# Performance work log

Measured on AMD Instinct MI355X. Metric: run time of the kernel, lower is better.

Reference implementation:

```python
import jax, jax.numpy as jnp
import numpy as np

B, L, H, HKV, D, E = 2, 2048, 8, 1, 256, 2048
SCALING = D ** -0.5


def rotate_half(x):
    x1, x2 = jnp.split(x, 2, axis=-1)
    return jnp.concatenate([-x2, x1], axis=-1)


def setup_inputs() -> dict:
    key = jax.random.key(0)
    ks = jax.random.split(key, 5)
    hidden_states = jax.random.normal(ks[0], (B, L, E), jnp.float32)
    attention_mask = jnp.zeros((B, 1, 1, L, L), jnp.float32)  # additive mask (all visible)
    # standard RoPE tables, shape [L, D]
    inv_freq = 1.0 / (10000.0 ** (jnp.arange(0, D, 2, dtype=jnp.float32) / D))
    freqs = jnp.arange(L, dtype=jnp.float32)[:, None] * inv_freq[None, :]
    emb = jnp.concatenate([freqs, freqs], axis=-1)
    cos, sin = jnp.cos(emb), jnp.sin(emb)
    s = 0.02
    Wq = jax.random.normal(ks[1], (H * D, E), jnp.float32) * s
    Wk = jax.random.normal(ks[2], (HKV * D, E), jnp.float32) * s
    Wv = jax.random.normal(ks[3], (HKV * D, E), jnp.float32) * s
    Wo = jax.random.normal(ks[4], (E, H * D), jnp.float32) * s
    return {"hidden_states": hidden_states, "attention_mask": attention_mask,
            "cos": cos, "sin": sin, "Wq": Wq, "Wk": Wk, "Wv": Wv, "Wo": Wo}


def reference(hidden_states, attention_mask, cos, sin, Wq, Wk, Wv, Wo):
    b, l, _ = hidden_states.shape
    q = jnp.einsum('ble,de->bld', hidden_states, Wq)
    k = jnp.einsum('ble,de->bld', hidden_states, Wk)
    v = jnp.einsum('ble,de->bld', hidden_states, Wv)
    # q: [B, L, 1, H, D] -> transpose(1,3) -> [B, H, 1, L, D]
    q = jnp.transpose(q.reshape(b, l, 1, H, D), (0, 3, 2, 1, 4))
    # k, v: [B, 1, L, Hkv, D] -> transpose(2,3) -> [B, 1, Hkv, L, D]
    k = jnp.transpose(k.reshape(b, 1, l, HKV, D), (0, 1, 3, 2, 4))
    v = jnp.transpose(v.reshape(b, 1, l, HKV, D), (0, 1, 3, 2, 4))
    # RoPE (cos/sin broadcast over leading dims)
    q = q * cos + rotate_half(q) * sin
    k = k * cos + rotate_half(k) * sin
    # scores: [B, H, Hkv, L, L]
    attn = jnp.matmul(q, jnp.swapaxes(k, -1, -2)) * SCALING
    attn = attn + attention_mask
    attn = jax.nn.softmax(attn.astype(jnp.float32), axis=-1)
    out = jnp.matmul(attn, v)                         # [B, H, Hkv, L, D]
    out = jnp.transpose(out, (0, 1, 3, 2, 4))         # [B, H, L, Hkv, D]
    out = out.reshape(b, l, H * D)                    # row-major reshape, as torch .reshape
    return jnp.einsum('bld,ed->ble', out, Wo)
```

## Files before the change

kernel.cpp:

```cpp
#include <hip/hip_runtime.h>

typedef unsigned short u16;
typedef __attribute__((ext_vector_type(8))) short short8;
typedef __attribute__((ext_vector_type(4))) float f32x4;

struct __align__(8) US4 { u16 x, y, z, w; };

__device__ __forceinline__ u16 f2bf(float x) {
  union { float f; unsigned u; } c; c.f = x;
  unsigned r = c.u + 0x7fffu + ((c.u >> 16) & 1u);
  return (u16)(r >> 16);
}
__device__ __forceinline__ float bf2f(u16 u) {
  union { unsigned u; float f; } c; c.u = ((unsigned)u) << 16;
  return c.f;
}
__device__ __forceinline__ void gload_lds16(const void* g, void* l) {
  __builtin_amdgcn_global_load_lds(
      (const __attribute__((address_space(1))) void*)g,
      (__attribute__((address_space(3))) void*)l, 16, 0, 0);
}
__device__ __forceinline__ f32x4 fzero4() {
  f32x4 z; z[0] = 0.f; z[1] = 0.f; z[2] = 0.f; z[3] = 0.f; return z;
}

__global__ __launch_bounds__(256) void cvt_all(
    const float* __restrict__ h, const float* __restrict__ wq,
    const float* __restrict__ wk, const float* __restrict__ wv,
    const float* __restrict__ wo, u16* __restrict__ Xbf,
    u16* __restrict__ Wqkv, u16* __restrict__ Wob) {
  int b = blockIdx.x;
  const float* s; u16* d; int off;
  if (b < 8192)       { s = h;  d = Xbf;            off = b; }
  else if (b < 12288) { s = wq; d = Wqkv;           off = b - 8192; }
  else if (b < 12800) { s = wk; d = Wqkv + 4194304; off = b - 12288; }
  else if (b < 13312) { s = wv; d = Wqkv + 4718592; off = b - 12800; }
  else                { s = wo; d = Wob;            off = b - 13312; }
  int i = (off * 256 + threadIdx.x) * 4;
  float4 v = *(const float4*)(s + i);
  US4 o = { f2bf(v.x), f2bf(v.y), f2bf(v.z), f2bf(v.w) };
  *(US4*)(d + i) = o;
}

template <int MODE>
__global__ __launch_bounds__(256) void gemm_nt(
    const u16* __restrict__ A, const u16* __restrict__ Bw,
    u16* __restrict__ q_out, u16* __restrict__ k_out, u16* __restrict__ v_out,
    float* __restrict__ c_out) {
  __shared__ u16 lA[128 * 32];
  __shared__ u16 lB[128 * 32];
  const int K = 2048;
  int t = threadIdx.x, w = t >> 6, lane = t & 63;
  int wm = w >> 1, wn = w & 1;
  int m0 = blockIdx.x * 128, n0 = blockIdx.y * 128;
  int g = lane >> 4, qi = lane & 15;

  f32x4 acc[4][4];
#pragma unroll
  for (int i = 0; i < 4; i++)
#pragma unroll
    for (int j = 0; j < 4; j++) acc[i][j] = fzero4();

  for (int k0 = 0; k0 < K; k0 += 32) {
#pragma unroll
    for (int i = 0; i < 2; i++) {
      int off = i * 4096 + w * 1024 + lane * 16;
      int row = off >> 6, cg = (off >> 4) & 3;
      gload_lds16(A + (size_t)(m0 + row) * K + k0 + cg * 8,
                  (char*)lA + i * 4096 + w * 1024);
      gload_lds16(Bw + (size_t)(n0 + row) * K + k0 + cg * 8,
                  (char*)lB + i * 4096 + w * 1024);
    }
    __syncthreads();
    short8 af[4], bfr[4];
#pragma unroll
    for (int f = 0; f < 4; f++) {
      int ra = wm * 64 + f * 16 + qi;
      int rb = wn * 64 + f * 16 + qi;
      int kb2 = g * 16;
      af[f] = *(const short8*)((const char*)lA + ra * 64 + kb2);
      bfr[f] = *(const short8*)((const char*)lB + rb * 64 + kb2);
    }
#pragma unroll
    for (int i = 0; i < 4; i++)
#pragma unroll
      for (int j = 0; j < 4; j++)
        acc[i][j] = __builtin_amdgcn_mfma_f32_16x16x32_bf16(af[i], bfr[j], acc[i][j], 0, 0, 0);
    __syncthreads();
  }

#pragma unroll
  for (int i = 0; i < 4; i++) {
#pragma unroll
    for (int j = 0; j < 4; j++) {
#pragma unroll
      for (int r = 0; r < 4; r++) {
        int m = m0 + wm * 64 + i * 16 + g * 4 + r;
        int n = n0 + wn * 64 + j * 16 + qi;
        float v = acc[i][j][r];
        if (MODE == 0) {
          int b = m >> 11, l = m & 2047;
          if (n < 2048) {
            int h = n >> 8, dd = n & 255;
            q_out[(((size_t)(b * 8 + h) * 2048) + l) * 256 + dd] = f2bf(v);
          } else if (n < 2304) {
            int dd = n - 2048;
            k_out[((size_t)b * 2048 + l) * 256 + dd] = f2bf(v);
          } else {
            int dd = n - 2304;
            v_out[((size_t)b * 256 + dd) * 2048 + l] = f2bf(v);
          }
        } else {
          c_out[(size_t)m * 2048 + n] = v;
        }
      }
    }
  }
}

__global__ __launch_bounds__(256) void rope_kernel(u16* __restrict__ q, u16* __restrict__ k,
                                                   const float* __restrict__ cosT,
                                                   const float* __restrict__ sinT) {
  int idx = blockIdx.x * 2 + (threadIdx.x >> 7);
  int d = threadIdx.x & 127;
  u16* ptr;
  int l;
  float sc;
  if (idx < 32768) { ptr = q + (size_t)idx * 256; l = idx & 2047; sc = 0.0625f; }
  else             { ptr = k + (size_t)(idx - 32768) * 256; l = (idx - 32768) & 2047; sc = 1.0f; }
  float x1 = bf2f(ptr[d]), x2 = bf2f(ptr[d + 128]);
  float c1 = cosT[l * 256 + d], s1 = sinT[l * 256 + d];
  float c2 = cosT[l * 256 + d + 128], s2 = sinT[l * 256 + d + 128];
  float o1 = (x1 * c1 - x2 * s1) * sc;
  float o2 = (x2 * c2 + x1 * s2) * sc;
  ptr[d] = f2bf(o1);
  ptr[d + 128] = f2bf(o2);
}

__global__ __launch_bounds__(256, 1) void flash_kernel(
    const u16* __restrict__ qr, const u16* __restrict__ kr,
    const u16* __restrict__ vt_g, u16* __restrict__ attnout) {
  __shared__ u16 kt[2][64 * 256];
  __shared__ u16 vt[2][256 * 64];
  __shared__ u16 pl[4][2048];

  int t = threadIdx.x, w = t >> 6, lane = t & 63;
  int qi = lane & 15, g = lane >> 4;
  int b = blockIdx.z, h = blockIdx.y;
  int bh = b * 8 + h;
  int l0 = blockIdx.x * 128 + w * 32;

  const u16* kb = kr + (size_t)b * (2048 * 256);
  const u16* vb = vt_g + (size_t)b * (256 * 2048);

  short8 qf[2][8];
#pragma unroll
  for (int qg = 0; qg < 2; qg++) {
    const u16* qbase = qr + ((size_t)bh * 2048 + l0 + qg * 16 + qi) * 256 + g * 8;
#pragma unroll
    for (int ks = 0; ks < 8; ks++) qf[qg][ks] = *(const short8*)(qbase + ks * 32);
  }

  f32x4 ot[16][2];
#pragma unroll
  for (int fd = 0; fd < 16; fd++) { ot[fd][0] = fzero4(); ot[fd][1] = fzero4(); }
  float mrow[2] = { -1e30f, -1e30f }, lrow[2] = { 0.f, 0.f };

  auto stage = [&](int buf, int kv) {
#pragma unroll
    for (int i = 0; i < 8; i++) {
      int off = i * 4096 + w * 1024 + lane * 16;
      int row = off >> 9, gc = (off >> 4) & 31;
      int gs = gc ^ (row & 7);
      gload_lds16(kb + (size_t)(kv + row) * 256 + gs * 8,
                  (char*)kt[buf] + i * 4096 + w * 1024);
    }
#pragma unroll
    for (int i = 0; i < 8; i++) {
      int off = i * 4096 + w * 1024 + lane * 16;
      int d = off >> 7, gc = (off >> 4) & 7;
      int gs = gc ^ (d & 7);
      gload_lds16(vb + (size_t)d * 2048 + kv + gs * 8,
                  (char*)vt[buf] + i * 4096 + w * 1024);
    }
  };

  stage(0, 0);
  __syncthreads();

  for (int tt = 0; tt < 32; ++tt) {
    int cur = tt & 1;
    if (tt < 31) stage(cur ^ 1, (tt + 1) * 64);

    f32x4 st[4][2];
    const char* kbase = (const char*)kt[cur];
#pragma unroll
    for (int f = 0; f < 4; f++) {
      st[f][0] = fzero4(); st[f][1] = fzero4();
      int row = f * 16 + qi;
#pragma unroll
      for (int ks = 0; ks < 8; ks++) {
        int slot = (4 * ks + g) ^ (row & 7);
        short8 kf = *(const short8*)(kbase + row * 512 + slot * 16);
        st[f][0] = __builtin_amdgcn_mfma_f32_16x16x32_bf16(kf, qf[0][ks], st[f][0], 0, 0, 0);
        st[f][1] = __builtin_amdgcn_mfma_f32_16x16x32_bf16(kf, qf[1][ks], st[f][1], 0, 0, 0);
      }
    }

#pragma unroll
    for (int qg = 0; qg < 2; qg++) {
      float tmax = -1e30f;
#pragma unroll
      for (int f = 0; f < 4; f++)
#pragma unroll
        for (int r = 0; r < 4; r++) tmax = fmaxf(tmax, st[f][qg][r]);
      tmax = fmaxf(tmax, __shfl_xor(tmax, 16));
      tmax = fmaxf(tmax, __shfl_xor(tmax, 32));
      float mnew = fmaxf(mrow[qg], tmax);
      float scale = __expf(mrow[qg] - mnew);
      float tsum = 0.f;
#pragma unroll
      for (int f = 0; f < 4; f++)
#pragma unroll
        for (int r = 0; r < 4; r++) {
          float p = __expf(st[f][qg][r] - mnew);
          st[f][qg][r] = p;
          tsum += p;
        }
      tsum += __shfl_xor(tsum, 16);
      tsum += __shfl_xor(tsum, 32);
      lrow[qg] = lrow[qg] * scale + tsum;
      mrow[qg] = mnew;
#pragma unroll
      for (int fd = 0; fd < 16; fd++)
#pragma unroll
        for (int r = 0; r < 4; r++) ot[fd][qg][r] *= scale;

      int qrow = qg * 16 + qi;
#pragma unroll
      for (int f = 0; f < 4; f++) {
        US4 pw = { f2bf(st[f][qg][0]), f2bf(st[f][qg][1]),
                   f2bf(st[f][qg][2]), f2bf(st[f][qg][3]) };
        int byte_ = (qrow * 128 + f * 32 + g * 8) ^ ((qi & 7) << 4);
        *(US4*)((char*)pl[w] + byte_) = pw;
      }
    }

    const char* vbase = (const char*)vt[cur];
#pragma unroll
    for (int s = 0; s < 2; s++) {
      int pb0 = ((0 * 16 + qi) * 128 + s * 64 + g * 16) ^ ((qi & 7) << 4);
      int pb1 = ((1 * 16 + qi) * 128 + s * 64 + g * 16) ^ ((qi & 7) << 4);
      short8 pf0 = *(const short8*)((const char*)pl[w] + pb0);
      short8 pf1 = *(const short8*)((const char*)pl[w] + pb1);
#pragma unroll
      for (int fd = 0; fd < 16; fd++) {
        int d = fd * 16 + qi;
        int slot = (s * 4 + g) ^ (d & 7);
        short8 vf = *(const short8*)(vbase + d * 128 + slot * 16);
        ot[fd][0] = __builtin_amdgcn_mfma_f32_16x16x32_bf16(vf, pf0, ot[fd][0], 0, 0, 0);
        ot[fd][1] = __builtin_amdgcn_mfma_f32_16x16x32_bf16(vf, pf1, ot[fd][1], 0, 0, 0);
      }
    }
    __syncthreads();
  }

#pragma unroll
  for (int qg = 0; qg < 2; qg++) {
    float inv = 1.f / lrow[qg];
    u16* ob = attnout + ((size_t)bh * 2048 + l0 + qg * 16 + qi) * 256;
#pragma unroll
    for (int fd = 0; fd < 16; fd++) {
      US4 o = { f2bf(ot[fd][qg][0] * inv), f2bf(ot[fd][qg][1] * inv),
                f2bf(ot[fd][qg][2] * inv), f2bf(ot[fd][qg][3] * inv) };
      *(US4*)(ob + fd * 16 + g * 4) = o;
    }
  }
}

extern "C" void kernel_launch(void* const* d_in, const int* in_sizes, int n_in,
                              void* d_out, int out_size, void* d_ws, size_t ws_size,
                              hipStream_t stream) {
  const float* hidden = (const float*)d_in[0];
  const float* cosT = (const float*)d_in[2];
  const float* sinT = (const float*)d_in[3];
  const float* Wq = (const float*)d_in[4];
  const float* Wk = (const float*)d_in[5];
  const float* Wv = (const float*)d_in[6];
  const float* Wo = (const float*)d_in[7];

  char* ws = (char*)d_ws;
  u16* Xbf  = (u16*)(ws + 0);
  u16* Wqkv = (u16*)(ws + 16777216);
  u16* Wob  = (u16*)(ws + 27262976);
  u16* qbuf = (u16*)(ws + 35651584);
  u16* kbuf = (u16*)(ws + 52428800);
  u16* vT   = (u16*)(ws + 54525952);
  u16* attn = (u16*)(ws + 56623104);
  float* out = (float*)d_out;

  cvt_all<<<17408, 256, 0, stream>>>(hidden, Wq, Wk, Wv, Wo, Xbf, Wqkv, Wob);
  gemm_nt<0><<<dim3(32, 20), 256, 0, stream>>>(Xbf, Wqkv, qbuf, kbuf, vT, nullptr);
  rope_kernel<<<18432, 256, 0, stream>>>(qbuf, kbuf, cosT, sinT);
  flash_kernel<<<dim3(16, 8, 2), 256, 0, stream>>>(qbuf, kbuf, vT, attn);
  gemm_nt<1><<<dim3(32, 16), 256, 0, stream>>>(attn, Wob, nullptr, nullptr, nullptr, out);
}
```

Measured before the change: 300.1 us.

## Split KV range across two wave groups in flash kernel with 32x32 MFMA

The attention kernel now launches 512 threads per block. Two groups of four waves each process half of the key/value sequence for the same 128 query rows, and their partial softmax states are merged through shared memory at the end. It also switches from 16x16x32 to 32x32x16 bf16 MFMA tiles, so each wave owns 32 query rows with a single score accumulator. Rescaling of the output accumulator is skipped when no lane's row max increases. The aim is more waves per CU for latency hiding and fewer MFMA and LDS fragment loads per useful flop, at the cost of about 144KB of LDS per block, an extra merge pass and an extra barrier.

```diff
diff --git a/kernel.cpp b/kernel.cpp
--- a/kernel.cpp
+++ b/kernel.cpp
@@ -3,6 +3,7 @@
 typedef unsigned short u16;
 typedef __attribute__((ext_vector_type(8))) short short8;
 typedef __attribute__((ext_vector_type(4))) float f32x4;
+typedef __attribute__((ext_vector_type(16))) float f32x16;
 
 struct __align__(8) US4 { u16 x, y, z, w; };
 
@@ -101,8 +102,8 @@
         if (MODE == 0) {
           int b = m >> 11, l = m & 2047;
           if (n < 2048) {
-            int h = n >> 8, dd = n & 255;
-            q_out[(((size_t)(b * 8 + h) * 2048) + l) * 256 + dd] = f2bf(v);
+            int hh = n >> 8, dd = n & 255;
+            q_out[(((size_t)(b * 8 + hh) * 2048) + l) * 256 + dd] = f2bf(v);
           } else if (n < 2304) {
             int dd = n - 2048;
             k_out[((size_t)b * 2048 + l) * 256 + dd] = f2bf(v);
@@ -137,144 +138,158 @@
   ptr[d + 128] = f2bf(o2);
 }
 
-__global__ __launch_bounds__(256, 1) void flash_kernel(
+__global__ __launch_bounds__(512, 2) void flash_kernel(
     const u16* __restrict__ qr, const u16* __restrict__ kr,
     const u16* __restrict__ vt_g, u16* __restrict__ attnout) {
-  __shared__ u16 kt[2][64 * 256];
-  __shared__ u16 vt[2][256 * 64];
-  __shared__ u16 pl[4][2048];
+  __shared__ __align__(16) char lds[147456];
 
   int t = threadIdx.x, w = t >> 6, lane = t & 63;
-  int qi = lane & 15, g = lane >> 4;
+  int lo5 = lane & 31, hi = lane >> 5;
+  int half = w >> 2, wl = w & 3;
   int b = blockIdx.z, h = blockIdx.y;
   int bh = b * 8 + h;
-  int l0 = blockIdx.x * 128 + w * 32;
+  int l0 = blockIdx.x * 128;
+  int qrow = l0 + wl * 32 + lo5;
 
   const u16* kb = kr + (size_t)b * (2048 * 256);
   const u16* vb = vt_g + (size_t)b * (256 * 2048);
-
-  short8 qf[2][8];
-#pragma unroll
-  for (int qg = 0; qg < 2; qg++) {
-    const u16* qbase = qr + ((size_t)bh * 2048 + l0 + qg * 16 + qi) * 256 + g * 8;
-#pragma unroll
-    for (int ks = 0; ks < 8; ks++) qf[qg][ks] = *(const short8*)(qbase + ks * 32);
-  }
-
-  f32x4 ot[16][2];
-#pragma unroll
-  for (int fd = 0; fd < 16; fd++) { ot[fd][0] = fzero4(); ot[fd][1] = fzero4(); }
-  float mrow[2] = { -1e30f, -1e30f }, lrow[2] = { 0.f, 0.f };
-
-  auto stage = [&](int buf, int kv) {
-#pragma unroll
-    for (int i = 0; i < 8; i++) {
-      int off = i * 4096 + w * 1024 + lane * 16;
-      int row = off >> 9, gc = (off >> 4) & 31;
-      int gs = gc ^ (row & 7);
-      gload_lds16(kb + (size_t)(kv + row) * 256 + gs * 8,
-                  (char*)kt[buf] + i * 4096 + w * 1024);
-    }
-#pragma unroll
-    for (int i = 0; i < 8; i++) {
-      int off = i * 4096 + w * 1024 + lane * 16;
-      int d = off >> 7, gc = (off >> 4) & 7;
-      int gs = gc ^ (d & 7);
-      gload_lds16(vb + (size_t)d * 2048 + kv + gs * 8,
-                  (char*)vt[buf] + i * 4096 + w * 1024);
+  char* unitbase = lds + half * 65536;
+  char* plw = lds + 131072 + w * 2048;
+  int kvbase = half * 1024;
+
+  short8 qf[16];
+  {
+    const u16* qb = qr + ((size_t)bh * 2048 + qrow) * 256 + hi * 8;
+#pragma unroll
+    for (int ks = 0; ks < 16; ks++) qf[ks] = *(const short8*)(qb + ks * 16);
+  }
+
+  f32x16 ot[8];
+#pragma unroll
+  for (int dv = 0; dv < 8; dv++)
+#pragma unroll
+    for (int r = 0; r < 16; r++) ot[dv][r] = 0.f;
+  float mrow = -1e30f, lrow = 0.f;
+
+  auto stage = [&](int buf, int it) {
+    char* unit = unitbase + buf * 32768;
+    int kvg = kvbase + it * 32;
+#pragma unroll
+    for (int i = 0; i < 4; i++) {
+      int dbase = i * 4096 + wl * 1024;
+      int off = dbase + lane * 16;
+      {
+        int row = off >> 9, slot = (off >> 4) & 31;
+        int ss = slot ^ (row & 7);
+        gload_lds16(kb + (size_t)(kvg + row) * 256 + ss * 8, unit + dbase);
+      }
+      {
+        int dd = off >> 6, slot = (off >> 4) & 3;
+        int ss = slot ^ ((dd >> 1) & 3);
+        gload_lds16(vb + (size_t)dd * 2048 + kvg + ss * 8, unit + 16384 + dbase);
+      }
     }
   };
 
   stage(0, 0);
   __syncthreads();
 
-  for (int tt = 0; tt < 32; ++tt) {
-    int cur = tt & 1;
-    if (tt < 31) stage(cur ^ 1, (tt + 1) * 64);
-
-    f32x4 st[4][2];
-    const char* kbase = (const char*)kt[cur];
-#pragma unroll
-    for (int f = 0; f < 4; f++) {
-      st[f][0] = fzero4(); st[f][1] = fzero4();
-      int row = f * 16 + qi;
-#pragma unroll
-      for (int ks = 0; ks < 8; ks++) {
-        int slot = (4 * ks + g) ^ (row & 7);
-        short8 kf = *(const short8*)(kbase + row * 512 + slot * 16);
-        st[f][0] = __builtin_amdgcn_mfma_f32_16x16x32_bf16(kf, qf[0][ks], st[f][0], 0, 0, 0);
-        st[f][1] = __builtin_amdgcn_mfma_f32_16x16x32_bf16(kf, qf[1][ks], st[f][1], 0, 0, 0);
-      }
-    }
-
-#pragma unroll
-    for (int qg = 0; qg < 2; qg++) {
-      float tmax = -1e30f;
-#pragma unroll
-      for (int f = 0; f < 4; f++)
-#pragma unroll
-        for (int r = 0; r < 4; r++) tmax = fmaxf(tmax, st[f][qg][r]);
-      tmax = fmaxf(tmax, __shfl_xor(tmax, 16));
-      tmax = fmaxf(tmax, __shfl_xor(tmax, 32));
-      float mnew = fmaxf(mrow[qg], tmax);
-      float scale = __expf(mrow[qg] - mnew);
-      float tsum = 0.f;
-#pragma unroll
-      for (int f = 0; f < 4; f++)
-#pragma unroll
-        for (int r = 0; r < 4; r++) {
-          float p = __expf(st[f][qg][r] - mnew);
-          st[f][qg][r] = p;
-          tsum += p;
-        }
-      tsum += __shfl_xor(tsum, 16);
-      tsum += __shfl_xor(tsum, 32);
-      lrow[qg] = lrow[qg] * scale + tsum;
-      mrow[qg] = mnew;
-#pragma unroll
-      for (int fd = 0; fd < 16; fd++)
-#pragma unroll
-        for (int r = 0; r < 4; r++) ot[fd][qg][r] *= scale;
-
-      int qrow = qg * 16 + qi;
-#pragma unroll
-      for (int f = 0; f < 4; f++) {
-        US4 pw = { f2bf(st[f][qg][0]), f2bf(st[f][qg][1]),
-                   f2bf(st[f][qg][2]), f2bf(st[f][qg][3]) };
-        int byte_ = (qrow * 128 + f * 32 + g * 8) ^ ((qi & 7) << 4);
-        *(US4*)((char*)pl[w] + byte_) = pw;
-      }
-    }
-
-    const char* vbase = (const char*)vt[cur];
-#pragma unroll
-    for (int s = 0; s < 2; s++) {
-      int pb0 = ((0 * 16 + qi) * 128 + s * 64 + g * 16) ^ ((qi & 7) << 4);
-      int pb1 = ((1 * 16 + qi) * 128 + s * 64 + g * 16) ^ ((qi & 7) << 4);
-      short8 pf0 = *(const short8*)((const char*)pl[w] + pb0);
-      short8 pf1 = *(const short8*)((const char*)pl[w] + pb1);
-#pragma unroll
-      for (int fd = 0; fd < 16; fd++) {
-        int d = fd * 16 + qi;
-        int slot = (s * 4 + g) ^ (d & 7);
-        short8 vf = *(const short8*)(vbase + d * 128 + slot * 16);
-        ot[fd][0] = __builtin_amdgcn_mfma_f32_16x16x32_bf16(vf, pf0, ot[fd][0], 0, 0, 0);
-        ot[fd][1] = __builtin_amdgcn_mfma_f32_16x16x32_bf16(vf, pf1, ot[fd][1], 0, 0, 0);
+  for (int it = 0; it < 32; ++it) {
+    int buf = it & 1;
+    if (it < 31) stage(buf ^ 1, it + 1);
+    char* unit = unitbase + buf * 32768;
+
+    f32x16 st;
+#pragma unroll
+    for (int r = 0; r < 16; r++) st[r] = 0.f;
+#pragma unroll
+    for (int ks = 0; ks < 16; ks++) {
+      int ss = (2 * ks + hi) ^ (lo5 & 7);
+      short8 kf = *(const short8*)(unit + lo5 * 512 + ss * 16);
+      st = __builtin_amdgcn_mfma_f32_32x32x16_bf16(kf, qf[ks], st, 0, 0, 0);
+    }
+
+    float tmax = st[0];
+#pragma unroll
+    for (int r = 1; r < 16; r++) tmax = fmaxf(tmax, st[r]);
+    tmax = fmaxf(tmax, __shfl_xor(tmax, 32));
+    if (__any(tmax > mrow)) {
+      float mnew = fmaxf(mrow, tmax);
+      float scale = __expf(mrow - mnew);
+#pragma unroll
+      for (int dv = 0; dv < 8; dv++)
+#pragma unroll
+        for (int r = 0; r < 16; r++) ot[dv][r] *= scale;
+      lrow *= scale;
+      mrow = mnew;
+    }
+    float tsum = 0.f;
+#pragma unroll
+    for (int r = 0; r < 16; r++) {
+      float p = __expf(st[r] - mrow);
+      st[r] = p;
+      tsum += p;
+    }
+    tsum += __shfl_xor(tsum, 32);
+    lrow += tsum;
+
+#pragma unroll
+    for (int r4 = 0; r4 < 4; r4++) {
+      US4 pw = { f2bf(st[4 * r4 + 0]), f2bf(st[4 * r4 + 1]),
+                 f2bf(st[4 * r4 + 2]), f2bf(st[4 * r4 + 3]) };
+      int byte_ = lo5 * 64 + ((r4 ^ ((lo5 >> 1) & 3)) << 4) + hi * 8;
+      *(US4*)(plw + byte_) = pw;
+    }
+
+#pragma unroll
+    for (int jks = 0; jks < 2; jks++) {
+      int ps = ((2 * jks + hi) ^ ((lo5 >> 1) & 3)) << 4;
+      short8 pf = *(const short8*)(plw + lo5 * 64 + ps);
+#pragma unroll
+      for (int dv = 0; dv < 8; dv++) {
+        int dd = dv * 32 + lo5;
+        int ss = (2 * jks + hi) ^ ((dd >> 1) & 3);
+        short8 vf = *(const short8*)(unit + 16384 + dd * 64 + ss * 16);
+        ot[dv] = __builtin_amdgcn_mfma_f32_32x32x16_bf16(vf, pf, ot[dv], 0, 0, 0);
       }
     }
     __syncthreads();
   }
 
-#pragma unroll
-  for (int qg = 0; qg < 2; qg++) {
-    float inv = 1.f / lrow[qg];
-    u16* ob = attnout + ((size_t)bh * 2048 + l0 + qg * 16 + qi) * 256;
-#pragma unroll
-    for (int fd = 0; fd < 16; fd++) {
-      US4 o = { f2bf(ot[fd][qg][0] * inv), f2bf(ot[fd][qg][1] * inv),
-                f2bf(ot[fd][qg][2] * inv), f2bf(ot[fd][qg][3] * inv) };
-      *(US4*)(ob + fd * 16 + g * 4) = o;
-    }
+  char* chunk = lds + wl * 32768;
+  float* mlx = (float*)(lds + 131072 + wl * 4096);
+  if (half == 0) {
+#pragma unroll
+    for (int dv = 0; dv < 8; dv++)
+#pragma unroll
+      for (int r4 = 0; r4 < 4; r4++) {
+        f32x4 v;
+        v[0] = ot[dv][4 * r4 + 0]; v[1] = ot[dv][4 * r4 + 1];
+        v[2] = ot[dv][4 * r4 + 2]; v[3] = ot[dv][4 * r4 + 3];
+        *(f32x4*)(chunk + ((dv * 4 + r4) * 64 + lane) * 16) = v;
+      }
+    mlx[lane * 2 + 0] = mrow;
+    mlx[lane * 2 + 1] = lrow;
+  }
+  __syncthreads();
+  if (half == 1) {
+    float mA = mlx[lane * 2 + 0], lA = mlx[lane * 2 + 1];
+    float m = fmaxf(mA, mrow);
+    float cA = __expf(mA - m), cB = __expf(mrow - m);
+    float linv = 1.f / (lA * cA + lrow * cB);
+    u16* ob = attnout + ((size_t)bh * 2048 + qrow) * 256;
+#pragma unroll
+    for (int dv = 0; dv < 8; dv++)
+#pragma unroll
+      for (int r4 = 0; r4 < 4; r4++) {
+        f32x4 oA = *(const f32x4*)(chunk + ((dv * 4 + r4) * 64 + lane) * 16);
+        US4 o;
+        o.x = f2bf((oA[0] * cA + ot[dv][4 * r4 + 0] * cB) * linv);
+        o.y = f2bf((oA[1] * cA + ot[dv][4 * r4 + 1] * cB) * linv);
+        o.z = f2bf((oA[2] * cA + ot[dv][4 * r4 + 2] * cB) * linv);
+        o.w = f2bf((oA[3] * cA + ot[dv][4 * r4 + 3] * cB) * linv);
+        *(US4*)(ob + dv * 32 + 8 * r4 + 4 * hi) = o;
+      }
   }
 }
 
@@ -302,6 +317,6 @@
   cvt_all<<<17408, 256, 0, stream>>>(hidden, Wq, Wk, Wv, Wo, Xbf, Wqkv, Wob);
   gemm_nt<0><<<dim3(32, 20), 256, 0, stream>>>(Xbf, Wqkv, qbuf, kbuf, vT, nullptr);
   rope_kernel<<<18432, 256, 0, stream>>>(qbuf, kbuf, cosT, sinT);
-  flash_kernel<<<dim3(16, 8, 2), 256, 0, stream>>>(qbuf, kbuf, vT, attn);
+  flash_kernel<<<dim3(16, 8, 2), 512, 0, stream>>>(qbuf, kbuf, vT, attn);
   gemm_nt<1><<<dim3(32, 16), 256, 0, stream>>>(attn, Wob, nullptr, nullptr, nullptr, out);
 }
```

Result: faster. 281.0 us (-6.4%).
